# Kernel tuning notes

Hardware: AMD Instinct MI355X
Metric: run time of the kernel (lower is better)

Reference implementation:

```python
import jax, jax.numpy as jnp
import numpy as np

N, C, H, W, NH = 2, 192, 256, 256, 6  # batch, channels, height, width, heads


def conv(x, w, groups=1):
    # NCHW conv, SAME padding, stride 1 (matches nn.Conv2d with padding=k//2)
    return jax.lax.conv_general_dilated(
        x, w, window_strides=(1, 1), padding='SAME',
        dimension_numbers=('NCHW', 'OIHW', 'NCHW'),
        feature_group_count=groups)


def setup_inputs() -> dict:
    key = jax.random.key(0)
    ks = jax.random.split(key, 5)
    x = jax.random.normal(ks[0], (N, C, H, W), jnp.float32)
    w1 = jax.random.normal(ks[1], (3 * C, C, 1, 1), jnp.float32) * 0.05   # 1x1 qkv proj
    w2 = jax.random.normal(ks[2], (3 * C, 1, 3, 3), jnp.float32) * 0.05   # depthwise 3x3
    w3 = jax.random.normal(ks[3], (3 * C, 1, 3, 3), jnp.float32) * 0.05   # depthwise 3x3
    factor = jnp.ones((1,), jnp.float32)                                   # learnable scale
    wf = jax.random.normal(ks[4], (C, C, 1, 1), jnp.float32) * 0.05       # final 1x1
    return {'x': x, 'w1': w1, 'w2': w2, 'w3': w3, 'factor': factor, 'wf': wf}


def reference(x, w1, w2, w3, factor, wf):
    n, c, h, w = x.shape
    dh = c // NH
    # conv-generated QKV: 1x1 -> depthwise 3x3 -> depthwise 3x3
    qkv = conv(conv(conv(x, w1), w2, groups=3 * c), w3, groups=3 * c)
    q, k, v = jnp.split(qkv, 3, axis=1)  # each [n, c, h, w]

    def rows(t):  # 'n (nh dh) h w -> (n nh h) w dh'  (row-wise axial attention)
        return t.reshape(n, NH, dh, h, w).transpose(0, 1, 3, 4, 2).reshape(n * NH * h, w, dh)

    q, k, v = rows(q), rows(k), rows(v)
    # L2-normalize along dh (F.normalize eps=1e-12 via clamp_min)
    q = q / jnp.maximum(jnp.linalg.norm(q, axis=-1, keepdims=True), 1e-12)
    k = k / jnp.maximum(jnp.linalg.norm(k, axis=-1, keepdims=True), 1e-12)
    scores = jnp.einsum('bqd,bkd->bqk', q, k) * factor[0]  # [(n nh h), w, w]
    attn = jax.nn.softmax(scores, axis=-1)
    out = jnp.einsum('bqk,bkd->bqd', attn, v)
    # '(n nh h) w dh -> n (nh dh) h w'
    out = out.reshape(n, NH, h, w, dh).transpose(0, 1, 4, 2, 3).reshape(n, c, h, w)
    return conv(out, wf)
```

## Files before the change

kernel.cpp:

```cpp
#include <hip/hip_runtime.h>
#include <hip/hip_bf16.h>
#include <math.h>

#define NB 2
#define CC 192
#define HH 256
#define WW 256
#define NHD 6
#define DH 32
#define C3 576

typedef __attribute__((ext_vector_type(8))) short bf16x8;
typedef __attribute__((ext_vector_type(4))) float f32x4;

__device__ __forceinline__ ushort f2b(float v) {
    __hip_bfloat16 b = __float2bfloat16(v);
    return *reinterpret_cast<ushort*>(&b);
}
__device__ __forceinline__ float b2f(ushort u) {
    __hip_bfloat16 b;
    *reinterpret_cast<ushort*>(&b) = u;
    return __bfloat162float(b);
}
__device__ __forceinline__ float bu(ushort u) {
    uint x = (uint)u << 16;
    return __uint_as_float(x);
}
__device__ __forceinline__ float exp2_fast(float x) {
#if __has_builtin(__builtin_amdgcn_exp2f)
    return __builtin_amdgcn_exp2f(x);
#else
    return exp2f(x);
#endif
}
__device__ __forceinline__ uint pk2(float x, float y) {
    return (__float_as_uint(y) & 0xFFFF0000u) | (__float_as_uint(x) >> 16);
}

__device__ __forceinline__ void gl_lds16(const void* g, void* l) {
    __builtin_amdgcn_global_load_lds((const __attribute__((address_space(1))) void*)g,
                                     (__attribute__((address_space(3))) void*)l, 16, 0, 0);
}

__global__ __launch_bounds__(256) void prep_w(const float* __restrict__ w1,
                                              const float* __restrict__ wf,
                                              ushort* __restrict__ Whi,
                                              ushort* __restrict__ Wlo) {
    int i = blockIdx.x * 256 + threadIdx.x;
    float v = (i < C3 * CC) ? w1[i] : wf[i - C3 * CC];
    ushort h = f2b(v);
    Whi[i] = h;
    Wlo[i] = f2b(v - b2f(h));
}

__global__ __launch_bounds__(256) void prep_xt(const float* __restrict__ x,
                                               ushort* __restrict__ Xhi,
                                               int n, int h0, int BH) {
    const int p0 = blockIdx.x * 64;
    const int gh = h0 - 2 + (p0 >> 8);
    const int wcol = p0 & 255;
    const int t = threadIdx.x;

    if (gh < 0 || gh >= HH) {
        uint* H = (uint*)(Xhi + (size_t)p0 * CC);
        for (int e = t; e < 64 * CC / 2; e += 256) H[e] = 0u;
        return;
    }

    __shared__ float xs[CC][65];
    const float* xb = x + ((size_t)n * CC) * (HH * WW) + (size_t)gh * WW + wcol;
    for (int e = t; e < CC * 16; e += 256) {
        int ic = e >> 4, j = e & 15;
        float4 v = *(const float4*)(xb + (size_t)ic * (HH * WW) + j * 4);
        xs[ic][j * 4 + 0] = v.x;
        xs[ic][j * 4 + 1] = v.y;
        xs[ic][j * 4 + 2] = v.z;
        xs[ic][j * 4 + 3] = v.w;
    }
    __syncthreads();

    const int r = t >> 2;
    const int k0 = (t & 3) * 48;
    uint* H = (uint*)(Xhi + ((size_t)p0 + r) * CC + k0);
    #pragma unroll
    for (int j = 0; j < 48; j += 2) {
        H[j >> 1] = (uint)f2b(xs[k0 + j][r]) | ((uint)f2b(xs[k0 + j + 1][r]) << 16);
    }
}

template<bool BSPLIT, bool OUTBF16>
__global__ __launch_bounds__(256) void gemm_split(const ushort* __restrict__ Whi,
                                                  const ushort* __restrict__ Wlo,
                                                  const ushort* __restrict__ Bhi,
                                                  const ushort* __restrict__ Blo,
                                                  void* __restrict__ Cout, int ldc,
                                                  int RS, int SS, int NM) {
    __shared__ ushort lA[2][64][64];
    __shared__ ushort lB[BSPLIT ? 2 : 1][128][64];

    const int bid = blockIdx.x;
    const int xcd = bid & 7;
    const int idx = bid >> 3;
    const int ptpx = (int)(gridDim.x >> 3) / NM;
    const int mtile = (idx % NM) * 64;
    const int ptile = (xcd * ptpx + idx / NM) * 128;

    const int t = threadIdx.x, wv = t >> 6, ln = t & 63;
    const int wm = wv >> 1, wn = wv & 1;

    f32x4 zero = {0.f, 0.f, 0.f, 0.f};
    f32x4 acc[2][4];
    #pragma unroll
    for (int fm = 0; fm < 2; ++fm)
        #pragma unroll
        for (int fn = 0; fn < 4; ++fn) acc[fm][fn] = zero;

    const int r8 = ln >> 3, s = ln & 7;
    const int CPW = BSPLIT ? 12 : 8;

    for (int kk = 0; kk < 3; ++kk) {
        const int k0 = kk * 64;
        #pragma unroll
        for (int ci = 0; ci < CPW; ++ci) {
            const int c = wv * CPW + ci;
            const ushort* g;
            void* l;
            if (c < 16) {
                const int pl = c >> 3, ch = c & 7;
                const int r = ch * 8 + r8;
                g = (pl ? Wlo : Whi) + (size_t)(mtile + r) * CC + k0 + ((s ^ (r & 7)) << 3);
                l = (void*)&lA[pl][ch * 8][0];
            } else {
                const int c2 = c - 16;
                const int pl = BSPLIT ? (c2 >> 4) : 0;
                const int ch = BSPLIT ? (c2 & 15) : c2;
                const int r = ch * 8 + r8;
                const int kq = k0 + ((s ^ (r & 7)) << 3);
                g = ((BSPLIT && pl) ? Blo : Bhi) + (size_t)(kq >> 5) * (size_t)SS
                                      + (size_t)(ptile + r) * (size_t)RS + (kq & 31);
                l = (void*)&lB[pl][ch * 8][0];
            }
            gl_lds16(g, l);
        }
        __syncthreads();

        #pragma unroll
        for (int ks = 0; ks < 2; ++ks) {
            bf16x8 ah[2], al[2], bh[4], bl[4];
            #pragma unroll
            for (int fm = 0; fm < 2; ++fm) {
                const int r = wm * 32 + fm * 16 + (ln & 15);
                const int col = (((ks * 4 + (ln >> 4)) ^ (r & 7)) << 3);
                ah[fm] = *(const bf16x8*)&lA[0][r][col];
                al[fm] = *(const bf16x8*)&lA[1][r][col];
            }
            #pragma unroll
            for (int fn = 0; fn < 4; ++fn) {
                const int r = wn * 64 + fn * 16 + (ln & 15);
                const int col = (((ks * 4 + (ln >> 4)) ^ (r & 7)) << 3);
                bh[fn] = *(const bf16x8*)&lB[0][r][col];
                if (BSPLIT) bl[fn] = *(const bf16x8*)&lB[1][r][col];
            }
            #pragma unroll
            for (int fm = 0; fm < 2; ++fm)
                #pragma unroll
                for (int fn = 0; fn < 4; ++fn) {
                    acc[fm][fn] = __builtin_amdgcn_mfma_f32_16x16x32_bf16(ah[fm], bh[fn], acc[fm][fn], 0, 0, 0);
                    if (BSPLIT)
                        acc[fm][fn] = __builtin_amdgcn_mfma_f32_16x16x32_bf16(ah[fm], bl[fn], acc[fm][fn], 0, 0, 0);
                    acc[fm][fn] = __builtin_amdgcn_mfma_f32_16x16x32_bf16(al[fm], bh[fn], acc[fm][fn], 0, 0, 0);
                }
        }
        __syncthreads();
    }

    #pragma unroll
    for (int fm = 0; fm < 2; ++fm)
        #pragma unroll
        for (int fn = 0; fn < 4; ++fn)
            #pragma unroll
            for (int r = 0; r < 4; ++r) {
                const int m = mtile + wm * 32 + fm * 16 + (ln >> 4) * 4 + r;
                const int p = ptile + wn * 64 + fn * 16 + (ln & 15);
                if (OUTBF16)
                    ((ushort*)Cout)[(size_t)m * ldc + p] = f2b(acc[fm][fn][r]);
                else
                    ((float*)Cout)[(size_t)m * ldc + p] = acc[fm][fn][r];
            }
}

struct RowH { float4 v; float l, r; };

__device__ __forceinline__ RowH k2_expand(ushort4 p, int ln) {
    RowH q;
    q.v = make_float4(bu(p.x), bu(p.y), bu(p.z), bu(p.w));
    q.l = __shfl_up(q.v.w, 1);
    q.r = __shfl_down(q.v.x, 1);
    if (ln == 0) q.l = 0.f;
    if (ln == 63) q.r = 0.f;
    return q;
}

__device__ __forceinline__ float4 k2_conv(const RowH& a, const RowH& b, const RowH& c,
                                          const float* w) {
    float4 o;
    o.x = fmaf(a.l,   w[0], fmaf(a.v.x, w[1], fmaf(a.v.y, w[2],
          fmaf(b.l,   w[3], fmaf(b.v.x, w[4], fmaf(b.v.y, w[5],
          fmaf(c.l,   w[6], fmaf(c.v.x, w[7], c.v.y * w[8]))))))));
    o.y = fmaf(a.v.x, w[0], fmaf(a.v.y, w[1], fmaf(a.v.z, w[2],
          fmaf(b.v.x, w[3], fmaf(b.v.y, w[4], fmaf(b.v.z, w[5],
          fmaf(c.v.x, w[6], fmaf(c.v.y, w[7], c.v.z * w[8]))))))));
    o.z = fmaf(a.v.y, w[0], fmaf(a.v.z, w[1], fmaf(a.v.w, w[2],
          fmaf(b.v.y, w[3], fmaf(b.v.z, w[4], fmaf(b.v.w, w[5],
          fmaf(c.v.y, w[6], fmaf(c.v.z, w[7], c.v.w * w[8]))))))));
    o.w = fmaf(a.v.z, w[0], fmaf(a.v.w, w[1], fmaf(a.r,   w[2],
          fmaf(b.v.z, w[3], fmaf(b.v.w, w[4], fmaf(b.r,   w[5],
          fmaf(c.v.z, w[6], fmaf(c.v.w, w[7], c.r * w[8]))))))));
    return o;
}

__device__ __forceinline__ RowH k2_mid(const RowH& a, const RowH& b, const RowH& c,
                                       const float* w, bool zero, int ln) {
    RowH m;
    if (zero) {
        m.v = make_float4(0.f, 0.f, 0.f, 0.f);
        m.l = 0.f; m.r = 0.f;
        return m;
    }
    m.v = k2_conv(a, b, c, w);
    m.l = __shfl_up(m.v.w, 1);
    m.r = __shfl_down(m.v.x, 1);
    if (ln == 0) m.l = 0.f;
    if (ln == 63) m.r = 0.f;
    return m;
}

__global__ __launch_bounds__(256) void k2_dwdw(const ushort* __restrict__ A,
                                               const float* __restrict__ w2,
                                               const float* __restrict__ w3,
                                               ushort* __restrict__ Bqk,
                                               ushort* __restrict__ Bvh,
                                               int h0, int BH, int strips) {
    const int SR = BH / strips;
    const int wv = threadIdx.x >> 6, ln = threadIdx.x & 63;
    const int gid = blockIdx.x * 4 + wv;
    const int c = gid / strips;
    const int s = gid - c * strips;
    const int r0 = s * SR;

    float w2c[9], w3c[9];
    #pragma unroll
    for (int i = 0; i < 9; ++i) { w2c[i] = w2[c * 9 + i]; w3c[i] = w3[c * 9 + i]; }

    const ushort* Ac = A + (size_t)c * (BH + 4) * WW + 4 * ln;

    RowH i0 = k2_expand(*(const ushort4*)(Ac + (size_t)(r0 + 0) * WW), ln);
    RowH i1 = k2_expand(*(const ushort4*)(Ac + (size_t)(r0 + 1) * WW), ln);
    RowH i2 = k2_expand(*(const ushort4*)(Ac + (size_t)(r0 + 2) * WW), ln);
    ushort4 pf = *(const ushort4*)(Ac + (size_t)(r0 + 3) * WW);
    RowH m0 = k2_mid(i0, i1, i2, w2c, (h0 + r0 - 1) < 0, ln);
    i0 = i1; i1 = i2; i2 = k2_expand(pf, ln);
    pf = *(const ushort4*)(Ac + (size_t)(r0 + 4) * WW);
    RowH m1 = k2_mid(i0, i1, i2, w2c, false, ln);

    if (c < 2 * CC) {
        ushort* Bc = Bqk + (size_t)c * BH * WW + 4 * ln;
        #pragma unroll 4
        for (int r = r0; r < r0 + SR; ++r) {
            i0 = i1; i1 = i2; i2 = k2_expand(pf, ln);
            const int rn = (r + 5 < BH + 4) ? r + 5 : BH + 3;
            pf = *(const ushort4*)(Ac + (size_t)rn * WW);
            RowH m2 = k2_mid(i0, i1, i2, w2c, (h0 + r + 1) >= HH, ln);
            float4 o = k2_conv(m0, m1, m2, w3c);
            ushort4 ob;
            ob.x = f2b(o.x); ob.y = f2b(o.y); ob.z = f2b(o.z); ob.w = f2b(o.w);
            *(ushort4*)(Bc + (size_t)r * WW) = ob;
            m0 = m1; m1 = m2;
        }
    } else {
        ushort* Bc = Bvh + (size_t)(c - 2 * CC) * BH * WW;
        const int kp4 = 32 * (ln >> 3) + 8 * (ln & 3) + 4 * ((ln >> 2) & 1);
        #pragma unroll 4
        for (int r = r0; r < r0 + SR; ++r) {
            i0 = i1; i1 = i2; i2 = k2_expand(pf, ln);
            const int rn = (r + 5 < BH + 4) ? r + 5 : BH + 3;
            pf = *(const ushort4*)(Ac + (size_t)rn * WW);
            RowH m2 = k2_mid(i0, i1, i2, w2c, (h0 + r + 1) >= HH, ln);
            float4 o = k2_conv(m0, m1, m2, w3c);
            uint2 ob;
            ob.x = (uint)f2b(o.x) | ((uint)f2b(o.y) << 16);
            ob.y = (uint)f2b(o.z) | ((uint)f2b(o.w) << 16);
            *(uint2*)(Bc + (size_t)r * WW + kp4) = ob;
            m0 = m1; m1 = m2;
        }
    }
}

__global__ __launch_bounds__(512, 4) void k3_attn_mfma(const ushort* __restrict__ Bqk,
                                                       const ushort* __restrict__ Bvh,
                                                       const float* __restrict__ factor,
                                                       ushort* __restrict__ Ohi, int BH) {
    const int r = blockIdx.x / NHD;
    const int head = blockIdx.x % NHD;
    const int t = threadIdx.x;
    const size_t plane = (size_t)BH * WW;

    __shared__ __align__(16) char arena[32768];
    ushort* Ksp = (ushort*)arena;
    ushort* Vt  = (ushort*)(arena + 16384);
    uint*   Oar = (uint*)arena;

    const int wv = t >> 6, ln = t & 63;
    const int hig = ln >> 4, lo16 = ln & 15;
    const float fsc = factor[0];
    const float L2E = 1.4426950408889634f;
    const float mb2 = fabsf(fsc) * L2E;

    #pragma unroll
    for (int it = 0; it < 2; ++it) {
        const int G = (wv * 2 + it) * 64 + ln;
        const int d = G >> 5, g = G & 31;
        const ushort* src = Bvh + ((size_t)(head * DH + d) * BH + r) * WW
                                + ((g ^ (d & 7)) << 3);
        gl_lds16(src, (void*)(Vt + (size_t)(wv * 2 + it) * 512));
    }

    float qv[2][8];
    #pragma unroll
    for (int c = 0; c < 2; ++c) {
        const int qrow = wv * 32 + c * 16 + lo16;
        const ushort* qb = Bqk + ((size_t)(head * DH + hig * 8)) * plane + (size_t)r * WW + qrow;
        #pragma unroll
        for (int j = 0; j < 8; ++j) qv[c][j] = bu(qb[(size_t)j * plane]);
    }

    if (t < 256) {
        const int row = t;
        const ushort* base = Bqk + ((size_t)(CC + head * DH)) * plane + (size_t)r * WW + row;
        float v[32];
        #pragma unroll
        for (int d = 0; d < 32; ++d) v[d] = bu(base[(size_t)d * plane]);
        float ss = 0.f;
        #pragma unroll
        for (int d = 0; d < 32; ++d) ss = fmaf(v[d], v[d], ss);
        const float inv = 1.f / fmaxf(sqrtf(ss), 1e-12f);
        const int sw = (row >> 1) & 3;
        #pragma unroll
        for (int gq = 0; gq < 4; ++gq) {
            uint hu[4];
            #pragma unroll
            for (int j = 0; j < 4; ++j) {
                float v0 = v[gq * 8 + 2 * j] * inv, v1 = v[gq * 8 + 2 * j + 1] * inv;
                hu[j] = (uint)f2b(v0) | ((uint)f2b(v1) << 16);
            }
            const int off = row * 32 + ((gq ^ sw) << 3);
            *(uint4*)&Ksp[off] = make_uint4(hu[0], hu[1], hu[2], hu[3]);
        }
    }
    __syncthreads();

    union { bf16x8 v; uint u[4]; } qh_[2];
    #pragma unroll
    for (int c = 0; c < 2; ++c) {
        float ssq = 0.f;
        #pragma unroll
        for (int j = 0; j < 8; ++j) ssq = fmaf(qv[c][j], qv[c][j], ssq);
        ssq += __shfl_xor(ssq, 16);
        ssq += __shfl_xor(ssq, 32);
        const float qinv = fsc * L2E / fmaxf(sqrtf(ssq), 1e-12f);
        #pragma unroll
        for (int j = 0; j < 8; j += 2) {
            float v0 = qv[c][j] * qinv, v1 = qv[c][j + 1] * qinv;
            qh_[c].u[j >> 1] = (uint)f2b(v0) | ((uint)f2b(v1) << 16);
        }
    }

    f32x4 osave[2][2];
    float invl[2];

    #pragma unroll
    for (int c = 0; c < 2; ++c) {
        f32x4 s[16];
        const f32x4 cinit = {-mb2, -mb2, -mb2, -mb2};
        __builtin_amdgcn_s_setprio(1);
        #pragma unroll
        for (int f = 0; f < 16; ++f) {
            const int krow = f * 16 + lo16;
            const int koff = krow * 32 + ((hig ^ ((krow >> 1) & 3)) << 3);
            const bf16x8 kh = *(const bf16x8*)&Ksp[koff];
            s[f] = __builtin_amdgcn_mfma_f32_16x16x32_bf16(kh, qh_[c].v, cinit, 0, 0, 0);
        }
        __builtin_amdgcn_s_setprio(0);

        float lsum = 0.f;
        #pragma unroll
        for (int f = 0; f < 16; ++f) {
            #pragma unroll
            for (int rr = 0; rr < 4; ++rr) {
                float p = exp2_fast(s[f][rr]);
                s[f][rr] = p;
                lsum += p;
            }
        }
        lsum += __shfl_xor(lsum, 16);
        lsum += __shfl_xor(lsum, 32);
        invl[c] = 1.f / lsum;

        uint pu[32];
        #pragma unroll
        for (int f = 0; f < 16; ++f) {
            pu[2 * f]     = pk2(s[f][0], s[f][1]);
            pu[2 * f + 1] = pk2(s[f][2], s[f][3]);
        }

        f32x4 o0a = {0,0,0,0}, o0b = {0,0,0,0}, o1a = {0,0,0,0}, o1b = {0,0,0,0};
        __builtin_amdgcn_s_setprio(1);
        #pragma unroll
        for (int st = 0; st < 8; ++st) {
            union { bf16x8 v; uint u[4]; } pb;
            pb.u[0] = pu[4 * st];     pb.u[1] = pu[4 * st + 1];
            pb.u[2] = pu[4 * st + 2]; pb.u[3] = pu[4 * st + 3];
            {
                const int drow = lo16;
                const int voff = drow * 256 + (((4 * st + hig) ^ (drow & 7)) << 3);
                const bf16x8 vh = *(const bf16x8*)&Vt[voff];
                f32x4& o = (st & 1) ? o0b : o0a;
                o = __builtin_amdgcn_mfma_f32_16x16x32_bf16(vh, pb.v, o, 0, 0, 0);
            }
            {
                const int drow = 16 + lo16;
                const int voff = drow * 256 + (((4 * st + hig) ^ (drow & 7)) << 3);
                const bf16x8 vh = *(const bf16x8*)&Vt[voff];
                f32x4& o = (st & 1) ? o1b : o1a;
                o = __builtin_amdgcn_mfma_f32_16x16x32_bf16(vh, pb.v, o, 0, 0, 0);
            }
        }
        __builtin_amdgcn_s_setprio(0);
        #pragma unroll
        for (int rr = 0; rr < 4; ++rr) { o0a[rr] += o0b[rr]; o1a[rr] += o1b[rr]; }
        osave[c][0] = o0a;
        osave[c][1] = o1a;
    }

    __syncthreads();

    #pragma unroll
    for (int c = 0; c < 2; ++c) {
        const int qrow = wv * 32 + c * 16 + lo16;
        #pragma unroll
        for (int fm = 0; fm < 2; ++fm) {
            const f32x4 o = osave[c][fm];
            const float s0 = o[0] * invl[c], s1 = o[1] * invl[c];
            const float s2 = o[2] * invl[c], s3 = o[3] * invl[c];
            const int dp = 8 * fm + 2 * hig;
            Oar[qrow * 20 + dp]     = (uint)f2b(s0) | ((uint)f2b(s1) << 16);
            Oar[qrow * 20 + dp + 1] = (uint)f2b(s2) | ((uint)f2b(s3) << 16);
        }
    }
    __syncthreads();

    if (t < 256) {
        const size_t obase = ((size_t)head * (size_t)BH * WW + (size_t)r * WW + t) * DH;
        uint4* dh_ = (uint4*)(Ohi + obase);
        const uint* srcH = &Oar[t * 20];
        #pragma unroll
        for (int i = 0; i < 4; ++i) dh_[i] = *(const uint4*)&srcH[i * 4];
    }
}

extern "C" void kernel_launch(void* const* d_in, const int* in_sizes, int n_in,
                              void* d_out, int out_size, void* d_ws, size_t ws_size,
                              hipStream_t stream) {
    const float* x      = (const float*)d_in[0];
    const float* w1     = (const float*)d_in[1];
    const float* w2     = (const float*)d_in[2];
    const float* w3     = (const float*)d_in[3];
    const float* factor = (const float*)d_in[4];
    const float* wf     = (const float*)d_in[5];
    float* out = (float*)d_out;

    const size_t SW = (size_t)(C3 + CC) * CC * 2 * sizeof(ushort);
    int BH = 256;
    while (BH > 32) {
        size_t SA_ = (size_t)C3 * (BH + 4) * WW * 2;
        size_t SB_ = (size_t)BH * WW * C3 * 2;
        size_t SX_ = (size_t)(BH + 4) * WW * CC * 2;
        size_t SO_ = (size_t)NHD * BH * WW * DH * 2;
        if (SA_ >= SO_ && SB_ >= SX_ && SA_ + SB_ + SW <= ws_size) break;
        BH >>= 1;
    }
    const size_t SA = (size_t)C3 * (BH + 4) * WW * 2;
    const size_t SB = (size_t)BH * WW * C3 * 2;

    ushort* A   = (ushort*)d_ws;
    char*  Breg = (char*)d_ws + SA;
    ushort* Bqk = (ushort*)Breg;
    ushort* Bvh = (ushort*)(Breg + (size_t)2 * CC * BH * WW * 2);
    ushort* Wsp = (ushort*)((char*)d_ws + SA + SB);
    ushort* Whi = Wsp;
    ushort* Wlo = Wsp + (size_t)(C3 + CC) * CC;

    ushort* Xhi = (ushort*)Breg;
    ushort* Ohi = A;

    prep_w<<<dim3((C3 + CC) * CC / 256), dim3(256), 0, stream>>>(w1, wf, Whi, Wlo);

    for (int n = 0; n < NB; ++n) {
        for (int h0 = 0; h0 < HH; h0 += BH) {
            const int strips = BH / 16;
            prep_xt<<<dim3((BH + 4) * (WW / 64)), dim3(256), 0, stream>>>(x, Xhi, n, h0, BH);
            gemm_split<false, true><<<dim3(((BH + 4) * WW / 128) * (C3 / 64)), dim3(256), 0, stream>>>(
                Whi, Wlo, Xhi, nullptr, (void*)A, (BH + 4) * WW, CC, DH, C3 / 64);
            k2_dwdw<<<dim3(C3 * strips / 4), dim3(256), 0, stream>>>(A, w2, w3, Bqk, Bvh, h0, BH, strips);
            k3_attn_mfma<<<dim3(NHD * BH), dim3(512), 0, stream>>>(Bqk, Bvh, factor, Ohi, BH);
            gemm_split<false, false><<<dim3((BH * WW / 128) * (CC / 64)), dim3(256), 0, stream>>>(
                Whi + (size_t)C3 * CC, Wlo + (size_t)C3 * CC, Ohi, nullptr,
                (void*)(out + ((size_t)n * CC) * HH * WW + (size_t)h0 * WW), HH * WW,
                DH, BH * WW * DH, CC / 64);
        }
    }
}
```

Measured before the change: 321.3 us.

## Interleave two batch images across fused heterogeneous kernels to overlap stages

Gives each of the two batch images its own workspace buffers and launches combined kernels. In each, blocks are assigned either to one image's stage (GEMM, depthwise conv, or attention) or to the other image's next stage, so compute-heavy and memory-heavy work run together and fewer launches are needed. The GEMM is rebuilt as a 512-thread block running two 256-thread tiles. The dropped split-B path and packed bf16 stores are minor cleanups. The cost is twice the workspace, which may force a smaller row band BH, and more complex block scheduling and occupancy.

```diff
diff --git a/kernel.cpp b/kernel.cpp
--- a/kernel.cpp
+++ b/kernel.cpp
@@ -36,10 +36,21 @@
 __device__ __forceinline__ uint pk2(float x, float y) {
     return (__float_as_uint(y) & 0xFFFF0000u) | (__float_as_uint(x) >> 16);
 }
-
 __device__ __forceinline__ void gl_lds16(const void* g, void* l) {
     __builtin_amdgcn_global_load_lds((const __attribute__((address_space(1))) void*)g,
                                      (__attribute__((address_space(3))) void*)l, 16, 0, 0);
+}
+
+__device__ __forceinline__ void pick(int pbid, int CA, int CB, int NA, int nB,
+                                     int TTH, int tailA, int& isA, int& idx) {
+    if (pbid >= TTH) {
+        isA = tailA;
+        idx = tailA ? (pbid - nB) : (pbid - NA);
+        return;
+    }
+    const int per = CA + CB, q = pbid / per, rm = pbid % per;
+    if (rm < CA) { isA = 1; idx = q * CA + rm; }
+    else         { isA = 0; idx = q * CB + (rm - CA); }
 }
 
 __global__ __launch_bounds__(256) void prep_w(const float* __restrict__ w1,
@@ -55,7 +66,11 @@
 
 __global__ __launch_bounds__(256) void prep_xt(const float* __restrict__ x,
                                                ushort* __restrict__ Xhi,
-                                               int n, int h0, int BH) {
+                                               int n0, int h0, int BH,
+                                               size_t XTIMG) {
+    const int n = n0 + blockIdx.y;
+    Xhi += (size_t)blockIdx.y * XTIMG;
+
     const int p0 = blockIdx.x * 64;
     const int gh = h0 - 2 + (p0 >> 8);
     const int wcol = p0 & 255;
@@ -88,24 +103,25 @@
     }
 }
 
-template<bool BSPLIT, bool OUTBF16>
-__global__ __launch_bounds__(256) void gemm_split(const ushort* __restrict__ Whi,
-                                                  const ushort* __restrict__ Wlo,
-                                                  const ushort* __restrict__ Bhi,
-                                                  const ushort* __restrict__ Blo,
-                                                  void* __restrict__ Cout, int ldc,
-                                                  int RS, int SS, int NM) {
-    __shared__ ushort lA[2][64][64];
-    __shared__ ushort lB[BSPLIT ? 2 : 1][128][64];
-
-    const int bid = blockIdx.x;
-    const int xcd = bid & 7;
-    const int idx = bid >> 3;
-    const int ptpx = (int)(gridDim.x >> 3) / NM;
-    const int mtile = (idx % NM) * 64;
-    const int ptile = (xcd * ptpx + idx / NM) * 128;
-
-    const int t = threadIdx.x, wv = t >> 6, ln = t & 63;
+template<bool OUTBF16>
+__device__ __forceinline__ void dev_gemm(int i, int h, int vt, char* smem,
+                                         const ushort* __restrict__ Whi,
+                                         const ushort* __restrict__ Wlo,
+                                         const ushort* __restrict__ Bhi,
+                                         void* __restrict__ Cout, int ldc,
+                                         int RS, int SS, int NM, int vpx) {
+    ushort (*lA)[64][64] = (ushort (*)[64][64])smem;
+    ushort (*lB)[64]     = (ushort (*)[64])(smem + 16384);
+
+    const int xcd = i & 7;
+    int idx2 = ((i >> 3) << 1) | h;
+    const bool live = idx2 < vpx;
+    if (!live) idx2 = 0;
+    const int ptpx = vpx / NM;
+    const int mtile = (idx2 % NM) * 64;
+    const int ptile = (xcd * ptpx + idx2 / NM) * 128;
+
+    const int wv = vt >> 6, ln = vt & 63;
     const int wm = wv >> 1, wn = wv & 1;
 
     f32x4 zero = {0.f, 0.f, 0.f, 0.f};
@@ -116,13 +132,12 @@
         for (int fn = 0; fn < 4; ++fn) acc[fm][fn] = zero;
 
     const int r8 = ln >> 3, s = ln & 7;
-    const int CPW = BSPLIT ? 12 : 8;
 
     for (int kk = 0; kk < 3; ++kk) {
         const int k0 = kk * 64;
         #pragma unroll
-        for (int ci = 0; ci < CPW; ++ci) {
-            const int c = wv * CPW + ci;
+        for (int ci = 0; ci < 8; ++ci) {
+            const int c = wv * 8 + ci;
             const ushort* g;
             void* l;
             if (c < 16) {
@@ -131,14 +146,12 @@
                 g = (pl ? Wlo : Whi) + (size_t)(mtile + r) * CC + k0 + ((s ^ (r & 7)) << 3);
                 l = (void*)&lA[pl][ch * 8][0];
             } else {
-                const int c2 = c - 16;
-                const int pl = BSPLIT ? (c2 >> 4) : 0;
-                const int ch = BSPLIT ? (c2 & 15) : c2;
+                const int ch = c - 16;
                 const int r = ch * 8 + r8;
                 const int kq = k0 + ((s ^ (r & 7)) << 3);
-                g = ((BSPLIT && pl) ? Blo : Bhi) + (size_t)(kq >> 5) * (size_t)SS
-                                      + (size_t)(ptile + r) * (size_t)RS + (kq & 31);
-                l = (void*)&lB[pl][ch * 8][0];
+                g = Bhi + (size_t)(kq >> 5) * (size_t)SS
+                        + (size_t)(ptile + r) * (size_t)RS + (kq & 31);
+                l = (void*)&lB[ch * 8][0];
             }
             gl_lds16(g, l);
         }
@@ -146,7 +159,7 @@
 
         #pragma unroll
         for (int ks = 0; ks < 2; ++ks) {
-            bf16x8 ah[2], al[2], bh[4], bl[4];
+            bf16x8 ah[2], al[2], bh[4];
             #pragma unroll
             for (int fm = 0; fm < 2; ++fm) {
                 const int r = wm * 32 + fm * 16 + (ln & 15);
@@ -158,35 +171,34 @@
             for (int fn = 0; fn < 4; ++fn) {
                 const int r = wn * 64 + fn * 16 + (ln & 15);
                 const int col = (((ks * 4 + (ln >> 4)) ^ (r & 7)) << 3);
-                bh[fn] = *(const bf16x8*)&lB[0][r][col];
-                if (BSPLIT) bl[fn] = *(const bf16x8*)&lB[1][r][col];
+                bh[fn] = *(const bf16x8*)&lB[r][col];
             }
             #pragma unroll
             for (int fm = 0; fm < 2; ++fm)
                 #pragma unroll
                 for (int fn = 0; fn < 4; ++fn) {
                     acc[fm][fn] = __builtin_amdgcn_mfma_f32_16x16x32_bf16(ah[fm], bh[fn], acc[fm][fn], 0, 0, 0);
-                    if (BSPLIT)
-                        acc[fm][fn] = __builtin_amdgcn_mfma_f32_16x16x32_bf16(ah[fm], bl[fn], acc[fm][fn], 0, 0, 0);
                     acc[fm][fn] = __builtin_amdgcn_mfma_f32_16x16x32_bf16(al[fm], bh[fn], acc[fm][fn], 0, 0, 0);
                 }
         }
         __syncthreads();
     }
 
-    #pragma unroll
-    for (int fm = 0; fm < 2; ++fm)
-        #pragma unroll
-        for (int fn = 0; fn < 4; ++fn)
+    if (live) {
+        #pragma unroll
+        for (int fm = 0; fm < 2; ++fm)
             #pragma unroll
-            for (int r = 0; r < 4; ++r) {
-                const int m = mtile + wm * 32 + fm * 16 + (ln >> 4) * 4 + r;
-                const int p = ptile + wn * 64 + fn * 16 + (ln & 15);
-                if (OUTBF16)
-                    ((ushort*)Cout)[(size_t)m * ldc + p] = f2b(acc[fm][fn][r]);
-                else
-                    ((float*)Cout)[(size_t)m * ldc + p] = acc[fm][fn][r];
-            }
+            for (int fn = 0; fn < 4; ++fn)
+                #pragma unroll
+                for (int r = 0; r < 4; ++r) {
+                    const int m = mtile + wm * 32 + fm * 16 + (ln >> 4) * 4 + r;
+                    const int p = ptile + wn * 64 + fn * 16 + (ln & 15);
+                    if (OUTBF16)
+                        ((ushort*)Cout)[(size_t)m * ldc + p] = f2b(acc[fm][fn][r]);
+                    else
+                        ((float*)Cout)[(size_t)m * ldc + p] = acc[fm][fn][r];
+                }
+    }
 }
 
 struct RowH { float4 v; float l, r; };
@@ -235,15 +247,14 @@
     return m;
 }
 
-__global__ __launch_bounds__(256) void k2_dwdw(const ushort* __restrict__ A,
-                                               const float* __restrict__ w2,
-                                               const float* __restrict__ w3,
-                                               ushort* __restrict__ Bqk,
-                                               ushort* __restrict__ Bvh,
-                                               int h0, int BH, int strips) {
+__device__ __forceinline__ void dev_k2(int gid, int ln,
+                                       const ushort* __restrict__ A,
+                                       const float* __restrict__ w2,
+                                       const float* __restrict__ w3,
+                                       ushort* __restrict__ Bqk,
+                                       ushort* __restrict__ Bvh,
+                                       int h0, int BH, int strips) {
     const int SR = BH / strips;
-    const int wv = threadIdx.x >> 6, ln = threadIdx.x & 63;
-    const int gid = blockIdx.x * 4 + wv;
     const int c = gid / strips;
     const int s = gid - c * strips;
     const int r0 = s * SR;
@@ -272,9 +283,10 @@
             pf = *(const ushort4*)(Ac + (size_t)rn * WW);
             RowH m2 = k2_mid(i0, i1, i2, w2c, (h0 + r + 1) >= HH, ln);
             float4 o = k2_conv(m0, m1, m2, w3c);
-            ushort4 ob;
-            ob.x = f2b(o.x); ob.y = f2b(o.y); ob.z = f2b(o.z); ob.w = f2b(o.w);
-            *(ushort4*)(Bc + (size_t)r * WW) = ob;
+            uint2 ob;
+            ob.x = pk2(o.x, o.y);
+            ob.y = pk2(o.z, o.w);
+            *(uint2*)(Bc + (size_t)r * WW) = ob;
             m0 = m1; m1 = m2;
         }
     } else {
@@ -296,19 +308,18 @@
     }
 }
 
-__global__ __launch_bounds__(512, 4) void k3_attn_mfma(const ushort* __restrict__ Bqk,
-                                                       const ushort* __restrict__ Bvh,
-                                                       const float* __restrict__ factor,
-                                                       ushort* __restrict__ Ohi, int BH) {
-    const int r = blockIdx.x / NHD;
-    const int head = blockIdx.x % NHD;
-    const int t = threadIdx.x;
+__device__ __forceinline__ void dev_k3(int idx, int t, char* smem,
+                                       const ushort* __restrict__ Bqk,
+                                       const ushort* __restrict__ Bvh,
+                                       const float* __restrict__ factor,
+                                       ushort* __restrict__ Ohi, int BH) {
+    const int r = idx / NHD;
+    const int head = idx % NHD;
     const size_t plane = (size_t)BH * WW;
 
-    __shared__ __align__(16) char arena[32768];
-    ushort* Ksp = (ushort*)arena;
-    ushort* Vt  = (ushort*)(arena + 16384);
-    uint*   Oar = (uint*)arena;
+    ushort* Ksp = (ushort*)smem;
+    ushort* Vt  = (ushort*)(smem + 16384);
+    uint*   Oar = (uint*)smem;
 
     const int wv = t >> 6, ln = t & 63;
     const int hig = ln >> 4, lo16 = ln & 15;
@@ -468,6 +479,57 @@
     }
 }
 
+__global__ __launch_bounds__(512) void fuse_k2_gemm(
+    const ushort* kA, const float* w2, const float* w3, ushort* kBqk, ushort* kBvh,
+    int h0, int BH, int strips,
+    const ushort* Whi, const ushort* Wlo, const ushort* gB, void* gC,
+    int ldc, int RS, int SS, int NM, int vpx,
+    int NA, int NBc, int TTH, int tailA) {
+    __shared__ __align__(16) char smem[65536];
+    int isA, idx;
+    pick(blockIdx.x, 8, 16, NA, NBc, TTH, tailA, isA, idx);
+    const int t = threadIdx.x;
+    if (isA) {
+        dev_k2(idx * 8 + (t >> 6), t & 63, kA, w2, w3, kBqk, kBvh, h0, BH, strips);
+    } else {
+        const int h = t >> 8;
+        dev_gemm<true>(idx, h, t & 255, smem + h * 32768, Whi, Wlo, gB, gC, ldc, RS, SS, NM, vpx);
+    }
+}
+
+__global__ __launch_bounds__(512) void fuse_k3_k2(
+    const ushort* aBqk, const ushort* aBvh, const float* factor, ushort* aO, int BH,
+    const ushort* kA, const float* w2, const float* w3, ushort* kBqk, ushort* kBvh,
+    int h0, int strips,
+    int NA, int NBc, int TTH, int tailA) {
+    __shared__ __align__(16) char smem[32768];
+    int isA, idx;
+    pick(blockIdx.x, 8, 8, NA, NBc, TTH, tailA, isA, idx);
+    const int t = threadIdx.x;
+    if (isA) {
+        dev_k3(idx, t, smem, aBqk, aBvh, factor, aO, BH);
+    } else {
+        dev_k2(idx * 8 + (t >> 6), t & 63, kA, w2, w3, kBqk, kBvh, h0, BH, strips);
+    }
+}
+
+__global__ __launch_bounds__(512) void fuse_gemm_k3(
+    const ushort* Whi, const ushort* Wlo, const ushort* gB, void* gC,
+    int ldc, int RS, int SS, int NM, int vpx,
+    const ushort* bBqk, const ushort* bBvh, const float* factor, ushort* bO, int BH,
+    int NA, int NBc, int TTH, int tailA) {
+    __shared__ __align__(16) char smem[65536];
+    int isA, idx;
+    pick(blockIdx.x, 8, 16, NA, NBc, TTH, tailA, isA, idx);
+    const int t = threadIdx.x;
+    if (isA) {
+        const int h = t >> 8;
+        dev_gemm<false>(idx, h, t & 255, smem + h * 32768, Whi, Wlo, gB, gC, ldc, RS, SS, NM, vpx);
+    } else {
+        dev_k3(idx, t, smem, bBqk, bBvh, factor, bO, BH);
+    }
+}
+
 extern "C" void kernel_launch(void* const* d_in, const int* in_sizes, int n_in,
                               void* d_out, int out_size, void* d_ws, size_t ws_size,
                               hipStream_t stream) {
@@ -480,43 +542,73 @@
     float* out = (float*)d_out;
 
     const size_t SW = (size_t)(C3 + CC) * CC * 2 * sizeof(ushort);
+
     int BH = 256;
     while (BH > 32) {
         size_t SA_ = (size_t)C3 * (BH + 4) * WW * 2;
         size_t SB_ = (size_t)BH * WW * C3 * 2;
-        size_t SX_ = (size_t)(BH + 4) * WW * CC * 2;
-        size_t SO_ = (size_t)NHD * BH * WW * DH * 2;
-        if (SA_ >= SO_ && SB_ >= SX_ && SA_ + SB_ + SW <= ws_size) break;
+        if (2 * (SA_ + SB_) + SW <= ws_size) break;
         BH >>= 1;
     }
     const size_t SA = (size_t)C3 * (BH + 4) * WW * 2;
     const size_t SB = (size_t)BH * WW * C3 * 2;
 
-    ushort* A   = (ushort*)d_ws;
-    char*  Breg = (char*)d_ws + SA;
-    ushort* Bqk = (ushort*)Breg;
-    ushort* Bvh = (ushort*)(Breg + (size_t)2 * CC * BH * WW * 2);
-    ushort* Wsp = (ushort*)((char*)d_ws + SA + SB);
-    ushort* Whi = Wsp;
-    ushort* Wlo = Wsp + (size_t)(C3 + CC) * CC;
-
-    ushort* Xhi = (ushort*)Breg;
-    ushort* Ohi = A;
+    ushort* A    = (ushort*)d_ws;
+    ushort* Breg = (ushort*)((char*)d_ws + 2 * SA);
+    ushort* Wsp  = (ushort*)((char*)d_ws + 2 * (SA + SB));
+    ushort* Whi  = Wsp;
+    ushort* Wlo  = Wsp + (size_t)(C3 + CC) * CC;
+    ushort* Wfhi = Whi + (size_t)C3 * CC;
+    ushort* Wflo = Wlo + (size_t)C3 * CC;
+
+    const size_t AIMG = SA / 2;
+    const size_t BIMG = SB / 2;
+    const size_t QKOFF = (size_t)2 * CC * BH * WW;
+
+    ushort* A0 = A;              ushort* A1 = A + AIMG;
+    ushort* X0 = Breg;           ushort* X1 = Breg + BIMG;
+    ushort* Bqk0 = Breg;         ushort* Bqk1 = Breg + BIMG;
+    ushort* Bvh0 = Bqk0 + QKOFF; ushort* Bvh1 = Bqk1 + QKOFF;
+    float*  out0 = out;          float*  out1 = out + (size_t)CC * HH * WW;
+
+    const int strips = BH / 16;
+    const int physK2 = C3 * strips / 8;
+    const int physK3 = NHD * BH;
+    const int nvb1 = ((BH + 4) * WW / 128) * (C3 / 64);
+    const int vpx1 = nvb1 / 8;
+    const int physG1 = 8 * ((vpx1 + 1) / 2);
+    const int ldc1 = (BH + 4) * WW;
+    const int nvb2 = (BH * WW / 128) * (CC / 64);
+    const int vpx2 = nvb2 / 8;
+    const int physG2 = 8 * ((vpx2 + 1) / 2);
+    const int SS2 = BH * WW * DH;
 
     prep_w<<<dim3((C3 + CC) * CC / 256), dim3(256), 0, stream>>>(w1, wf, Whi, Wlo);
 
-    for (int n = 0; n < NB; ++n) {
-        for (int h0 = 0; h0 < HH; h0 += BH) {
-            const int strips = BH / 16;
-            prep_xt<<<dim3((BH + 4) * (WW / 64)), dim3(256), 0, stream>>>(x, Xhi, n, h0, BH);
-            gemm_split<false, true><<<dim3(((BH + 4) * WW / 128) * (C3 / 64)), dim3(256), 0, stream>>>(
-                Whi, Wlo, Xhi, nullptr, (void*)A, (BH + 4) * WW, CC, DH, C3 / 64);
-            k2_dwdw<<<dim3(C3 * strips / 4), dim3(256), 0, stream>>>(A, w2, w3, Bqk, Bvh, h0, BH, strips);
-            k3_attn_mfma<<<dim3(NHD * BH), dim3(512), 0, stream>>>(Bqk, Bvh, factor, Ohi, BH);
-            gemm_split<false, false><<<dim3((BH * WW / 128) * (CC / 64)), dim3(256), 0, stream>>>(
-                Whi + (size_t)C3 * CC, Wlo + (size_t)C3 * CC, Ohi, nullptr,
-                (void*)(out + ((size_t)n * CC) * HH * WW + (size_t)h0 * WW), HH * WW,
-                DH, BH * WW * DH, CC / 64);
-        }
-    }
-}
+    for (int h0 = 0; h0 < HH; h0 += BH) {
+        prep_xt<<<dim3((BH + 4) * (WW / 64), 2), dim3(256), 0, stream>>>(
+            x, Breg, 0, h0, BH, BIMG);
+        fuse_k2_gemm<<<dim3(physG1), dim3(512), 0, stream>>>(
+            A1, w2, w3, Bqk1, Bvh1, h0, BH, strips,
+            Whi, Wlo, X0, (void*)A0, ldc1, CC, DH, C3 / 64, vpx1,
+            0, physG1, 0, 0);
+        fuse_k2_gemm<<<dim3(physK2 + physG1), dim3(512), 0, stream>>>(
+            A0, w2, w3, Bqk0, Bvh0, h0, BH, strips,
+            Whi, Wlo, X1, (void*)A1, ldc1, CC, DH, C3 / 64, vpx1,
+            physK2, physG1, (physK2 / 8) * 24, 0);
+        fuse_k3_k2<<<dim3(physK3 + physK2), dim3(512), 0, stream>>>(
+            Bqk0, Bvh0, factor, A0, BH,
+            A1, w2, w3, Bqk1, Bvh1, h0, strips,
+            physK3, physK2, (physK2 / 8) * 16, 1);
+        fuse_gemm_k3<<<dim3(physG2 + physK3), dim3(512), 0, stream>>>(
+            Wfhi, Wflo, A0, (void*)(out0 + (size_t)h0 * WW), HH * WW,
+            DH, SS2, CC / 64, vpx2,
+            Bqk1, Bvh1, factor, A1, BH,
+            physG2, physK3, physG2 + physK3, 0);
+        fuse_gemm_k3<<<dim3(physG2), dim3(512), 0, stream>>>(
+            Wfhi, Wflo, A1, (void*)(out1 + (size_t)h0 * WW), HH * WW,
+            DH, SS2, CC / 64, vpx2,
+            Bqk1, Bvh1, factor, A1, BH,
+            physG2, 0, 0, 1);
+    }
+}
```

After: 321.7 us. Within noise of the previous version (+0.1%).
